# Optimization experiments

Hardware: AMD Instinct MI355X
Metric: run time of the kernel (lower is better)

Reference implementation:

```python
import jax, jax.numpy as jnp
import numpy as np

DELTA = 10.0
EPS = 1e-08
THRESHOLD = 0.9
STEEPNESS = 10.0


def setup_inputs() -> dict:
    key = jax.random.key(0)
    k1, k2 = jax.random.split(key)
    B, T2, T1, F = 16, 2048, 512, 128
    mels = jax.random.normal(k1, (B, T2, F), dtype=jnp.float32)
    alpha = jax.random.uniform(k2, (B, T2, T1), dtype=jnp.float32)
    mel_mask = jnp.ones((B, T2), dtype=jnp.int32)
    text_mask = jnp.ones((B, T1), dtype=jnp.int32)
    return {"mels": mels, "alpha": alpha, "mel_mask": mel_mask, "text_mask": text_mask}


def reference(mels, alpha, mel_mask, text_mask):
    B, T2, F = mels.shape
    T1 = text_mask.shape[-1]
    audio_mask = mel_mask.astype(bool)
    txt_mask = text_mask.astype(bool)
    am_f = audio_mask.astype(alpha.dtype)  # [B, T2]
    tm_f = txt_mask.astype(alpha.dtype)    # [B, T1]

    # index vector p: [B, T1]
    p = jnp.broadcast_to(jnp.arange(T1, dtype=alpha.dtype), (B, T1))

    # cosine similarity between consecutive frames (F.normalize: x / max(||x||, 1e-12))
    norm = jnp.maximum(jnp.linalg.norm(mels, axis=-1, keepdims=True), 1e-12)
    z_norm = mels / norm
    cosine_sim = jnp.sum(z_norm[:, :-1] * z_norm[:, 1:], axis=-1)  # [B, T2-1]
    activity = jax.nn.sigmoid(STEEPNESS * (THRESHOLD - cosine_sim))
    activity = jnp.concatenate([jnp.ones((B, 1), dtype=activity.dtype), activity], axis=-1)
    activity = activity * am_f

    # soft monotonic index via gated cumsum of alpha-proposal increments
    imv_proposal = jnp.einsum('bts,bs->bt', alpha, p)  # [B, T2]
    delta_prop = jnp.concatenate(
        [jnp.zeros((B, 1), dtype=imv_proposal.dtype), jnp.diff(imv_proposal, axis=-1)], axis=-1)
    eff_delta = jnp.clip(delta_prop * activity, 0.0, 1.0)
    imv = jnp.cumsum(eff_delta, axis=-1) * am_f

    # rescale so last valid frame maps to last phoneme index
    last_idx = jnp.maximum(audio_mask.sum(-1).astype(jnp.int32) - 1, 0)  # [B]
    last_val = jnp.maximum(jnp.take_along_axis(imv, last_idx[:, None], axis=1)[:, 0], 1e-06)
    text_len = txt_mask.sum(-1).astype(imv.dtype)
    scale = jnp.maximum(text_len - 1.0, 0.0) / last_val
    imv = imv * scale[:, None] * am_f

    # gamma: masked softmax over phonemes of -delta * (imv - p)^2
    dist_sq = (imv[:, :, None] - p[:, None, :]) ** 2  # [B, T2, T1]
    logits = jnp.where(txt_mask[:, None, :], -DELTA * dist_sq, -1e9)
    gamma = jax.nn.softmax(logits, axis=-1) * am_f[:, :, None]

    # durations: soft mass per phoneme
    durations = jnp.sum(gamma * am_f[:, :, None], axis=1) * tm_f  # [B, T1]

    # attention-pooling of mel frames onto phonemes
    w = jnp.swapaxes(gamma, 1, 2) * am_f[:, None, :]  # [B, T1, T2]
    w = w / (jnp.sum(w, axis=-1, keepdims=True) + EPS)
    aligned_mels = jnp.einsum('bst,btf->bsf', w, mels) * tm_f[:, :, None]  # [B, T1, F]
    return aligned_mels, durations, imv
```

## Files before the change

kernel.cpp:

```cpp
#include <hip/hip_runtime.h>
#include <math.h>
#include <cstddef>

#define B_  16
#define T2_ 2048
#define T1_ 512
#define F_  128

constexpr float DELTA_C  = 10.0f;
constexpr float EPS_C    = 1e-8f;
constexpr float THRESH_C = 0.9f;
constexpr float STEEP_C  = 10.0f;

typedef float f4v __attribute__((ext_vector_type(4)));

__global__ __launch_bounds__(256) void actprop_kernel(const float* __restrict__ mels,
                                                      const float* __restrict__ alpha,
                                                      const int* __restrict__ mel_mask,
                                                      float* __restrict__ act,
                                                      float* __restrict__ prop) {
    int wid  = (int)((blockIdx.x * blockDim.x + threadIdx.x) >> 6);
    int lane = threadIdx.x & 63;
    if (wid >= B_ * T2_) return;
    int t = wid % T2_;

    const f4v* row = (const f4v*)(alpha + (size_t)wid * T1_);
    f4v v0 = __builtin_nontemporal_load(&row[lane]);
    f4v v1 = __builtin_nontemporal_load(&row[lane + 64]);

    float d = 0.f, n0 = 0.f, n1 = 0.f;
    if (t > 0) {
        float2 x = ((const float2*)(mels + (size_t)(wid - 1) * F_))[lane];
        float2 y = ((const float2*)(mels + (size_t)wid * F_))[lane];
        d  = x.x * y.x + x.y * y.y;
        n0 = x.x * x.x + x.y * x.y;
        n1 = y.x * y.x + y.y * y.y;
    }

    float fL = (float)(lane * 4);
    float psum = v0.x * fL + v0.y * (fL + 1.f) + v0.z * (fL + 2.f) + v0.w * (fL + 3.f)
               + v1.x * (fL + 256.f) + v1.y * (fL + 257.f) + v1.z * (fL + 258.f) + v1.w * (fL + 259.f);

    for (int off = 32; off > 0; off >>= 1) {
        psum += __shfl_xor(psum, off, 64);
        d    += __shfl_xor(d,    off, 64);
        n0   += __shfl_xor(n0,   off, 64);
        n1   += __shfl_xor(n1,   off, 64);
    }

    if (lane == 0) {
        float a_val;
        if (t == 0) {
            a_val = 1.0f;
        } else {
            float cs = d / (fmaxf(sqrtf(n0), 1e-12f) * fmaxf(sqrtf(n1), 1e-12f));
            a_val = 1.0f / (1.0f + __expf(-STEEP_C * (THRESH_C - cs)));
        }
        act[wid]  = a_val * (float)mel_mask[wid];
        prop[wid] = psum;
    }
}

__global__ __launch_bounds__(256) void scan_kernel(const float* __restrict__ prop,
                                                   const float* __restrict__ act,
                                                   const int* __restrict__ mel_mask,
                                                   const int* __restrict__ text_mask,
                                                   float* __restrict__ imv_out,
                                                   float2* __restrict__ packed,
                                                   int2* __restrict__ bounds) {
    int b    = blockIdx.x;
    int tid  = threadIdx.x;
    int wave = tid >> 6, lane = tid & 63;
    __shared__ float s_imv[T2_];
    __shared__ float s_wsum[4];
    __shared__ int   s_am4[4], s_tm4[4];
    __shared__ int   s_tm[T1_];

    const float* pr = prop + (size_t)b * T2_;
    const float* ac = act  + (size_t)b * T2_;
    const int*   mm = mel_mask  + (size_t)b * T2_;
    const int*   tm = text_mask + (size_t)b * T1_;

    int tmv0 = tm[tid], tmv1 = tm[tid + 256];
    s_tm[tid] = tmv0; s_tm[tid + 256] = tmv1;

    float e[8];
    int   mmv[8];
    int t0 = tid * 8;
    int am_local = 0;
    float run = 0.0f;
    for (int i = 0; i < 8; i++) {
        int t = t0 + i;
        float d = (t == 0) ? 0.0f : (pr[t] - pr[t - 1]) * ac[t];
        d = fminf(fmaxf(d, 0.0f), 1.0f);
        run += d;
        e[i] = run;
        mmv[i] = mm[t];
        am_local += mmv[i];
    }
    int tm_local = tmv0 + tmv1;
    for (int off = 32; off > 0; off >>= 1) {
        am_local += __shfl_xor(am_local, off, 64);
        tm_local += __shfl_xor(tm_local, off, 64);
    }
    if (lane == 0) { s_am4[wave] = am_local; s_tm4[wave] = tm_local; }

    float v = run;
    for (int off = 1; off < 64; off <<= 1) {
        float u = __shfl_up(v, off, 64);
        if (lane >= off) v += u;
    }
    if (lane == 63) s_wsum[wave] = v;
    __syncthreads();

    float woff = 0.0f;
    for (int w = 0; w < 4; w++) woff += (w < wave) ? s_wsum[w] : 0.0f;
    float excl = woff + v - run;
    for (int i = 0; i < 8; i++) {
        int t = t0 + i;
        s_imv[t] = (e[i] + excl) * (float)mmv[i];
    }
    __syncthreads();

    int am_total = s_am4[0] + s_am4[1] + s_am4[2] + s_am4[3];
    int tm_total = s_tm4[0] + s_tm4[1] + s_tm4[2] + s_tm4[3];
    int last_idx = max(am_total - 1, 0);
    float last_val = fmaxf(s_imv[last_idx], 1e-6f);
    float scale = fmaxf((float)tm_total - 1.0f, 0.0f) / last_val;
    __syncthreads();

    for (int i = 0; i < 8; i++) {
        int t = t0 + i;
        int valid = mmv[i];
        float vv = s_imv[t] * scale * (float)valid;
        imv_out[(size_t)b * T2_ + t] = vv;
        int c = (int)floorf(vv);
        float Z = 0.0f;
        for (int s = c - 2; s <= c + 3; s++) {
            if (s >= 0 && s < T1_ && s_tm[s]) {
                float dd = vv - (float)s;
                Z += __expf(-DELTA_C * dd * dd);
            }
        }
        Z = fmaxf(Z, 1e-30f);
        float key = valid ? vv : 3.0e4f;
        float2 pk = {key, valid ? (1.0f / Z) : 0.0f};
        packed[(size_t)b * T2_ + t] = pk;
        s_imv[t] = key;
    }
    __syncthreads();

    for (int k = 0; k < 2; k++) {
        int s = tid + k * 256;
        float lov = (float)s - 3.0f, hiv = (float)s + 3.0f;
        int lo = 0, hi = T2_;
        while (lo < hi) { int mid = (lo + hi) >> 1; if (s_imv[mid] >= lov) hi = mid; else lo = mid + 1; }
        int st = lo;
        hi = T2_;
        while (lo < hi) { int mid = (lo + hi) >> 1; if (s_imv[mid] > hiv) hi = mid; else lo = mid + 1; }
        int2 be = {st, lo};
        bounds[(size_t)b * T1_ + s] = be;
    }
}

__global__ __launch_bounds__(256) void pool_kernel(const float* __restrict__ mels,
                                                   const int* __restrict__ text_mask,
                                                   const float2* __restrict__ packed,
                                                   const int2* __restrict__ bounds,
                                                   float* __restrict__ aligned,
                                                   float* __restrict__ dur) {
    int wid  = (int)((blockIdx.x * blockDim.x + threadIdx.x) >> 6);
    int lane = threadIdx.x & 63;
    if (wid >= B_ * (T1_ / 2)) return;
    int b = wid >> 8, s0 = (wid & 255) * 2;
    float fs0 = (float)s0, fs1 = fs0 + 1.0f;

    const float2* pk   = packed + (size_t)b * T2_;
    const float2* mel2 = (const float2*)(mels + (size_t)b * T2_ * F_);
    int2 b0 = bounds[(size_t)b * T1_ + s0];
    int2 b1 = bounds[(size_t)b * T1_ + s0 + 1];
    int t_lo = b0.x, t_hi = b1.y;

    float ax0 = 0.f, ay0 = 0.f, g0s = 0.f;
    float ax1 = 0.f, ay1 = 0.f, g1s = 0.f;
    int t = t_lo;
    for (; t + 2 <= t_hi; t += 2) {
        float2 p0 = pk[t], p1 = pk[t + 1];
        float2 m0 = mel2[(size_t)t * 64 + lane];
        float2 m1 = mel2[(size_t)(t + 1) * 64 + lane];
        float d00 = p0.x - fs0, d01 = p0.x - fs1;
        float d10 = p1.x - fs0, d11 = p1.x - fs1;
        float g00 = __expf(-DELTA_C * d00 * d00) * p0.y;
        float g01 = __expf(-DELTA_C * d01 * d01) * p0.y;
        float g10 = __expf(-DELTA_C * d10 * d10) * p1.y;
        float g11 = __expf(-DELTA_C * d11 * d11) * p1.y;
        g0s += g00 + g10; g1s += g01 + g11;
        ax0 += g00 * m0.x + g10 * m1.x;  ay0 += g00 * m0.y + g10 * m1.y;
        ax1 += g01 * m0.x + g11 * m1.x;  ay1 += g01 * m0.y + g11 * m1.y;
    }
    for (; t < t_hi; t++) {
        float2 p = pk[t];
        float2 m = mel2[(size_t)t * 64 + lane];
        float d0 = p.x - fs0, d1 = p.x - fs1;
        float ga = __expf(-DELTA_C * d0 * d0) * p.y;
        float gb = __expf(-DELTA_C * d1 * d1) * p.y;
        g0s += ga; g1s += gb;
        ax0 += ga * m.x; ay0 += ga * m.y;
        ax1 += gb * m.x; ay1 += gb * m.y;
    }

    float tm0 = (float)text_mask[(size_t)b * T1_ + s0];
    float tm1 = (float)text_mask[(size_t)b * T1_ + s0 + 1];
    float inv0 = tm0 / (g0s + EPS_C);
    float inv1 = tm1 / (g1s + EPS_C);
    float2 o0 = {ax0 * inv0, ay0 * inv0};
    float2 o1 = {ax1 * inv1, ay1 * inv1};
    ((float2*)(aligned + ((size_t)b * T1_ + s0) * F_))[lane] = o0;
    ((float2*)(aligned + ((size_t)b * T1_ + s0 + 1) * F_))[lane] = o1;
    if (lane == 0) {
        dur[(size_t)b * T1_ + s0]     = g0s * tm0;
        dur[(size_t)b * T1_ + s0 + 1] = g1s * tm1;
    }
}

extern "C" void kernel_launch(void* const* d_in, const int* in_sizes, int n_in,
                              void* d_out, int out_size, void* d_ws, size_t ws_size,
                              hipStream_t stream) {
    const float* mels      = (const float*)d_in[0];
    const float* alpha     = (const float*)d_in[1];
    const int*   mel_mask  = (const int*)d_in[2];
    const int*   text_mask = (const int*)d_in[3];

    float* out     = (float*)d_out;
    float* aligned = out;
    float* dur     = out + (size_t)B_ * T1_ * F_;
    float* imv     = dur + (size_t)B_ * T1_;

    float*  ws     = (float*)d_ws;
    float*  act    = ws;
    float*  prop   = ws + (size_t)B_ * T2_;
    float2* packed = (float2*)(ws + 2 * (size_t)B_ * T2_);
    int2*   bounds = (int2*)(ws + 4 * (size_t)B_ * T2_);

    dim3 blk(256);
    actprop_kernel<<<(B_ * T2_) / 4, blk, 0, stream>>>(mels, alpha, mel_mask, act, prop);
    scan_kernel   <<<B_,            blk, 0, stream>>>(prop, act, mel_mask, text_mask, imv, packed, bounds);
    pool_kernel   <<<(B_ * T1_ / 2) / 4, blk, 0, stream>>>(mels, text_mask, packed, bounds, aligned, dur);
}
```

Baseline: 132.8 us.

## Remap work: four rows per wave in actprop, wider scan block, split-wave pooling

The actprop kernel now handles four alpha rows per wave, with 16 lanes per row and eight vector loads per lane, which cuts reduction shuffles and grid size. The scan kernel runs 512 threads per batch with four elements per thread, and the pooling kernel splits each wave into two halves that process alternate frames using float4 mel loads, then merges them with a single shuffle. The goal is more memory-level parallelism and fewer wasted lanes and shuffles in the bandwidth-bound alpha pass. The cost is more registers per lane and some predicated idle work in the pooling tail.

```diff
diff --git a/kernel.cpp b/kernel.cpp
--- a/kernel.cpp
+++ b/kernel.cpp
@@ -19,36 +19,54 @@
                                                       const int* __restrict__ mel_mask,
                                                       float* __restrict__ act,
                                                       float* __restrict__ prop) {
-    int wid  = (int)((blockIdx.x * blockDim.x + threadIdx.x) >> 6);
+    int wv   = (int)((blockIdx.x * blockDim.x + threadIdx.x) >> 6);
     int lane = threadIdx.x & 63;
-    if (wid >= B_ * T2_) return;
-    int t = wid % T2_;
-
-    const f4v* row = (const f4v*)(alpha + (size_t)wid * T1_);
-    f4v v0 = __builtin_nontemporal_load(&row[lane]);
-    f4v v1 = __builtin_nontemporal_load(&row[lane + 64]);
-
-    float d = 0.f, n0 = 0.f, n1 = 0.f;
-    if (t > 0) {
-        float2 x = ((const float2*)(mels + (size_t)(wid - 1) * F_))[lane];
-        float2 y = ((const float2*)(mels + (size_t)wid * F_))[lane];
-        d  = x.x * y.x + x.y * y.y;
-        n0 = x.x * x.x + x.y * x.y;
-        n1 = y.x * y.x + y.y * y.y;
-    }
-
-    float fL = (float)(lane * 4);
-    float psum = v0.x * fL + v0.y * (fL + 1.f) + v0.z * (fL + 2.f) + v0.w * (fL + 3.f)
-               + v1.x * (fL + 256.f) + v1.y * (fL + 257.f) + v1.z * (fL + 258.f) + v1.w * (fL + 259.f);
-
-    for (int off = 32; off > 0; off >>= 1) {
+    int il   = lane & 15;
+    int r    = wv * 4 + (lane >> 4);
+    int t    = r & (T2_ - 1);
+
+    const f4v* arow = (const f4v*)(alpha + (size_t)r * T1_);
+    f4v a0 = __builtin_nontemporal_load(&arow[il]);
+    f4v a1 = __builtin_nontemporal_load(&arow[il + 16]);
+    f4v a2 = __builtin_nontemporal_load(&arow[il + 32]);
+    f4v a3 = __builtin_nontemporal_load(&arow[il + 48]);
+    f4v a4 = __builtin_nontemporal_load(&arow[il + 64]);
+    f4v a5 = __builtin_nontemporal_load(&arow[il + 80]);
+    f4v a6 = __builtin_nontemporal_load(&arow[il + 96]);
+    f4v a7 = __builtin_nontemporal_load(&arow[il + 112]);
+
+    int rm = (t == 0) ? r : (r - 1);
+    const f4v* my = (const f4v*)(mels + (size_t)r  * F_);
+    const f4v* mx = (const f4v*)(mels + (size_t)rm * F_);
+    f4v y0 = my[il * 2], y1 = my[il * 2 + 1];
+    f4v x0 = mx[il * 2], x1 = mx[il * 2 + 1];
+
+    float d  = x0.x*y0.x + x0.y*y0.y + x0.z*y0.z + x0.w*y0.w
+             + x1.x*y1.x + x1.y*y1.y + x1.z*y1.z + x1.w*y1.w;
+    float n0 = x0.x*x0.x + x0.y*x0.y + x0.z*x0.z + x0.w*x0.w
+             + x1.x*x1.x + x1.y*x1.y + x1.z*x1.z + x1.w*x1.w;
+    float n1 = y0.x*y0.x + y0.y*y0.y + y0.z*y0.z + y0.w*y0.w
+             + y1.x*y1.x + y1.y*y1.y + y1.z*y1.z + y1.w*y1.w;
+
+    float fb = (float)(il * 4);
+    float psum;
+    psum  = a0.x*(fb      ) + a0.y*(fb +   1.f) + a0.z*(fb +   2.f) + a0.w*(fb +   3.f);
+    psum += a1.x*(fb+ 64.f) + a1.y*(fb +  65.f) + a1.z*(fb +  66.f) + a1.w*(fb +  67.f);
+    psum += a2.x*(fb+128.f) + a2.y*(fb + 129.f) + a2.z*(fb + 130.f) + a2.w*(fb + 131.f);
+    psum += a3.x*(fb+192.f) + a3.y*(fb + 193.f) + a3.z*(fb + 194.f) + a3.w*(fb + 195.f);
+    psum += a4.x*(fb+256.f) + a4.y*(fb + 257.f) + a4.z*(fb + 258.f) + a4.w*(fb + 259.f);
+    psum += a5.x*(fb+320.f) + a5.y*(fb + 321.f) + a5.z*(fb + 322.f) + a5.w*(fb + 323.f);
+    psum += a6.x*(fb+384.f) + a6.y*(fb + 385.f) + a6.z*(fb + 386.f) + a6.w*(fb + 387.f);
+    psum += a7.x*(fb+448.f) + a7.y*(fb + 449.f) + a7.z*(fb + 450.f) + a7.w*(fb + 451.f);
+
+    for (int off = 8; off > 0; off >>= 1) {
         psum += __shfl_xor(psum, off, 64);
         d    += __shfl_xor(d,    off, 64);
         n0   += __shfl_xor(n0,   off, 64);
         n1   += __shfl_xor(n1,   off, 64);
     }
 
-    if (lane == 0) {
+    if (il == 0) {
         float a_val;
         if (t == 0) {
             a_val = 1.0f;
@@ -56,12 +74,12 @@
             float cs = d / (fmaxf(sqrtf(n0), 1e-12f) * fmaxf(sqrtf(n1), 1e-12f));
             a_val = 1.0f / (1.0f + __expf(-STEEP_C * (THRESH_C - cs)));
         }
-        act[wid]  = a_val * (float)mel_mask[wid];
-        prop[wid] = psum;
-    }
-}
-
-__global__ __launch_bounds__(256) void scan_kernel(const float* __restrict__ prop,
+        act[r]  = a_val * (float)mel_mask[r];
+        prop[r] = psum;
+    }
+}
+
+__global__ __launch_bounds__(512) void scan_kernel(const float* __restrict__ prop,
                                                    const float* __restrict__ act,
                                                    const int* __restrict__ mel_mask,
                                                    const int* __restrict__ text_mask,
@@ -72,8 +90,8 @@
     int tid  = threadIdx.x;
     int wave = tid >> 6, lane = tid & 63;
     __shared__ float s_imv[T2_];
-    __shared__ float s_wsum[4];
-    __shared__ int   s_am4[4], s_tm4[4];
+    __shared__ float s_wsum[8];
+    __shared__ int   s_am8[8], s_tm8[8];
     __shared__ int   s_tm[T1_];
 
     const float* pr = prop + (size_t)b * T2_;
@@ -81,29 +99,29 @@
     const int*   mm = mel_mask  + (size_t)b * T2_;
     const int*   tm = text_mask + (size_t)b * T1_;
 
-    int tmv0 = tm[tid], tmv1 = tm[tid + 256];
-    s_tm[tid] = tmv0; s_tm[tid + 256] = tmv1;
-
-    float e[8];
-    int   mmv[8];
-    int t0 = tid * 8;
+    int tmv = tm[tid];
+    s_tm[tid] = tmv;
+
+    float e[4];
+    int   mmv[4];
+    int t0 = tid * 4;
     int am_local = 0;
     float run = 0.0f;
-    for (int i = 0; i < 8; i++) {
+    for (int i = 0; i < 4; i++) {
         int t = t0 + i;
-        float d = (t == 0) ? 0.0f : (pr[t] - pr[t - 1]) * ac[t];
-        d = fminf(fmaxf(d, 0.0f), 1.0f);
-        run += d;
+        float dd = (t == 0) ? 0.0f : (pr[t] - pr[t - 1]) * ac[t];
+        dd = fminf(fmaxf(dd, 0.0f), 1.0f);
+        run += dd;
         e[i] = run;
         mmv[i] = mm[t];
         am_local += mmv[i];
     }
-    int tm_local = tmv0 + tmv1;
+    int tm_local = tmv;
     for (int off = 32; off > 0; off >>= 1) {
         am_local += __shfl_xor(am_local, off, 64);
         tm_local += __shfl_xor(tm_local, off, 64);
     }
-    if (lane == 0) { s_am4[wave] = am_local; s_tm4[wave] = tm_local; }
+    if (lane == 0) { s_am8[wave] = am_local; s_tm8[wave] = tm_local; }
 
     float v = run;
     for (int off = 1; off < 64; off <<= 1) {
@@ -114,22 +132,22 @@
     __syncthreads();
 
     float woff = 0.0f;
-    for (int w = 0; w < 4; w++) woff += (w < wave) ? s_wsum[w] : 0.0f;
+    for (int w = 0; w < 8; w++) woff += (w < wave) ? s_wsum[w] : 0.0f;
     float excl = woff + v - run;
-    for (int i = 0; i < 8; i++) {
+    for (int i = 0; i < 4; i++) {
         int t = t0 + i;
         s_imv[t] = (e[i] + excl) * (float)mmv[i];
     }
     __syncthreads();
 
-    int am_total = s_am4[0] + s_am4[1] + s_am4[2] + s_am4[3];
-    int tm_total = s_tm4[0] + s_tm4[1] + s_tm4[2] + s_tm4[3];
+    int am_total = 0, tm_total = 0;
+    for (int w = 0; w < 8; w++) { am_total += s_am8[w]; tm_total += s_tm8[w]; }
     int last_idx = max(am_total - 1, 0);
     float last_val = fmaxf(s_imv[last_idx], 1e-6f);
     float scale = fmaxf((float)tm_total - 1.0f, 0.0f) / last_val;
     __syncthreads();
 
-    for (int i = 0; i < 8; i++) {
+    for (int i = 0; i < 4; i++) {
         int t = t0 + i;
         int valid = mmv[i];
         float vv = s_imv[t] * scale * (float)valid;
@@ -150,8 +168,8 @@
     }
     __syncthreads();
 
-    for (int k = 0; k < 2; k++) {
-        int s = tid + k * 256;
+    {
+        int s = tid;
         float lov = (float)s - 3.0f, hiv = (float)s + 3.0f;
         int lo = 0, hi = T2_;
         while (lo < hi) { int mid = (lo + hi) >> 1; if (s_imv[mid] >= lov) hi = mid; else lo = mid + 1; }
@@ -173,54 +191,57 @@
     int lane = threadIdx.x & 63;
     if (wid >= B_ * (T1_ / 2)) return;
     int b = wid >> 8, s0 = (wid & 255) * 2;
+    int half = lane >> 5, hl = lane & 31;
     float fs0 = (float)s0, fs1 = fs0 + 1.0f;
 
     const float2* pk   = packed + (size_t)b * T2_;
-    const float2* mel2 = (const float2*)(mels + (size_t)b * T2_ * F_);
+    const f4v*    mel4 = (const f4v*)(mels + (size_t)b * T2_ * F_);
     int2 b0 = bounds[(size_t)b * T1_ + s0];
     int2 b1 = bounds[(size_t)b * T1_ + s0 + 1];
     int t_lo = b0.x, t_hi = b1.y;
 
-    float ax0 = 0.f, ay0 = 0.f, g0s = 0.f;
-    float ax1 = 0.f, ay1 = 0.f, g1s = 0.f;
-    int t = t_lo;
-    for (; t + 2 <= t_hi; t += 2) {
-        float2 p0 = pk[t], p1 = pk[t + 1];
-        float2 m0 = mel2[(size_t)t * 64 + lane];
-        float2 m1 = mel2[(size_t)(t + 1) * 64 + lane];
-        float d00 = p0.x - fs0, d01 = p0.x - fs1;
-        float d10 = p1.x - fs0, d11 = p1.x - fs1;
-        float g00 = __expf(-DELTA_C * d00 * d00) * p0.y;
-        float g01 = __expf(-DELTA_C * d01 * d01) * p0.y;
-        float g10 = __expf(-DELTA_C * d10 * d10) * p1.y;
-        float g11 = __expf(-DELTA_C * d11 * d11) * p1.y;
-        g0s += g00 + g10; g1s += g01 + g11;
-        ax0 += g00 * m0.x + g10 * m1.x;  ay0 += g00 * m0.y + g10 * m1.y;
-        ax1 += g01 * m0.x + g11 * m1.x;  ay1 += g01 * m0.y + g11 * m1.y;
-    }
-    for (; t < t_hi; t++) {
-        float2 p = pk[t];
-        float2 m = mel2[(size_t)t * 64 + lane];
+    float ax0 = 0.f, ay0 = 0.f, az0 = 0.f, aw0 = 0.f, g0s = 0.f;
+    float ax1 = 0.f, ay1 = 0.f, az1 = 0.f, aw1 = 0.f, g1s = 0.f;
+    for (int t = t_lo; t < t_hi; t += 2) {
+        int  tl = t + half;
+        bool on = tl < t_hi;
+        int  ts = on ? tl : t;
+        float2 p = pk[ts];
+        f4v    m = mel4[(size_t)ts * 32 + hl];
         float d0 = p.x - fs0, d1 = p.x - fs1;
-        float ga = __expf(-DELTA_C * d0 * d0) * p.y;
-        float gb = __expf(-DELTA_C * d1 * d1) * p.y;
-        g0s += ga; g1s += gb;
-        ax0 += ga * m.x; ay0 += ga * m.y;
-        ax1 += gb * m.x; ay1 += gb * m.y;
-    }
+        float g0 = on ? __expf(-DELTA_C * d0 * d0) * p.y : 0.0f;
+        float g1 = on ? __expf(-DELTA_C * d1 * d1) * p.y : 0.0f;
+        g0s += g0; g1s += g1;
+        ax0 += g0 * m.x; ay0 += g0 * m.y; az0 += g0 * m.z; aw0 += g0 * m.w;
+        ax1 += g1 * m.x; ay1 += g1 * m.y; az1 += g1 * m.z; aw1 += g1 * m.w;
+    }
+
+    g0s += __shfl_xor(g0s, 32, 64);
+    g1s += __shfl_xor(g1s, 32, 64);
+    ax0 += __shfl_xor(ax0, 32, 64);
+    ay0 += __shfl_xor(ay0, 32, 64);
+    az0 += __shfl_xor(az0, 32, 64);
+    aw0 += __shfl_xor(aw0, 32, 64);
+    ax1 += __shfl_xor(ax1, 32, 64);
+    ay1 += __shfl_xor(ay1, 32, 64);
+    az1 += __shfl_xor(az1, 32, 64);
+    aw1 += __shfl_xor(aw1, 32, 64);
 
     float tm0 = (float)text_mask[(size_t)b * T1_ + s0];
     float tm1 = (float)text_mask[(size_t)b * T1_ + s0 + 1];
     float inv0 = tm0 / (g0s + EPS_C);
     float inv1 = tm1 / (g1s + EPS_C);
-    float2 o0 = {ax0 * inv0, ay0 * inv0};
-    float2 o1 = {ax1 * inv1, ay1 * inv1};
-    ((float2*)(aligned + ((size_t)b * T1_ + s0) * F_))[lane] = o0;
-    ((float2*)(aligned + ((size_t)b * T1_ + s0 + 1) * F_))[lane] = o1;
-    if (lane == 0) {
-        dur[(size_t)b * T1_ + s0]     = g0s * tm0;
-        dur[(size_t)b * T1_ + s0 + 1] = g1s * tm1;
-    }
+
+    f4v out;
+    if (half == 0) {
+        out.x = ax0 * inv0; out.y = ay0 * inv0; out.z = az0 * inv0; out.w = aw0 * inv0;
+    } else {
+        out.x = ax1 * inv1; out.y = ay1 * inv1; out.z = az1 * inv1; out.w = aw1 * inv1;
+    }
+    float* obase = aligned + ((size_t)b * T1_ + s0 + half) * F_;
+    ((f4v*)obase)[hl] = out;
+    if (lane == 0)  dur[(size_t)b * T1_ + s0]     = g0s * tm0;
+    if (lane == 32) dur[(size_t)b * T1_ + s0 + 1] = g1s * tm1;
 }
 
 extern "C" void kernel_launch(void* const* d_in, const int* in_sizes, int n_in,
@@ -242,8 +263,7 @@
     float2* packed = (float2*)(ws + 2 * (size_t)B_ * T2_);
     int2*   bounds = (int2*)(ws + 4 * (size_t)B_ * T2_);
 
-    dim3 blk(256);
-    actprop_kernel<<<(B_ * T2_) / 4, blk, 0, stream>>>(mels, alpha, mel_mask, act, prop);
-    scan_kernel   <<<B_,            blk, 0, stream>>>(prop, act, mel_mask, text_mask, imv, packed, bounds);
-    pool_kernel   <<<(B_ * T1_ / 2) / 4, blk, 0, stream>>>(mels, text_mask, packed, bounds, aligned, dur);
-}
+    actprop_kernel<<<(B_ * T2_) / 16, dim3(256), 0, stream>>>(mels, alpha, mel_mask, act, prop);
+    scan_kernel   <<<B_,              dim3(512), 0, stream>>>(prop, act, mel_mask, text_mask, imv, packed, bounds);
+    pool_kernel   <<<(B_ * T1_ / 2) / 4, dim3(256), 0, stream>>>(mels, text_mask, packed, bounds, aligned, dur);
+}
```

Result: faster. 128.4 us (-3.4%).
